# Optimization experiments

Hardware: AMD Instinct MI355X
Metric: run time of the kernel (lower is better)

## Reference

```python
import jax, jax.numpy as jnp
import numpy as np

B, S, D_MODEL = 1, 2048, 2048
N_HEADS, N_KV_HEADS, D_HEAD = 16, 4, 128
ROTARY_DIM, ROTARY_BASE = 128, 10000.0
ATTN_SCALE = float(np.sqrt(D_HEAD))
REPEAT = N_HEADS // N_KV_HEADS


def _sin_cos_rotary(n_ctx, rotary_dim, base):
    # TransformerLens calculate_sin_cos_rotary, rotary_adjacent_pairs=False:
    # freq repeated as 'd -> (2 d)'
    pos = jnp.arange(n_ctx, dtype=jnp.float32)
    dim = jnp.arange(rotary_dim // 2, dtype=jnp.float32)
    freq = base ** (dim / (rotary_dim / 2))
    freq = jnp.concatenate([freq, freq])  # (2 d)
    angles = pos[:, None] / freq[None, :]  # [n_ctx, rotary_dim]
    return jnp.sin(angles), jnp.cos(angles)


def _rotate_every_two_half(x):
    # rotate_half for non-adjacent pairs: [-x2, x1]
    d = x.shape[-1]
    return jnp.concatenate([-x[..., d // 2:], x[..., : d // 2]], axis=-1)


def _apply_rotary(x, sin, cos):
    # x: [batch, pos, head, d_head]; sin/cos: [n_ctx, rotary_dim]
    p = x.shape[1]
    s = sin[:p][:, None, :]  # [pos, 1, rotary_dim]
    c = cos[:p][:, None, :]
    x_rot = x[..., :ROTARY_DIM]
    x_pass = x[..., ROTARY_DIM:]
    x_rotated = x_rot * c + _rotate_every_two_half(x_rot) * s
    return jnp.concatenate([x_rotated, x_pass], axis=-1)


def setup_inputs() -> dict:
    key = jax.random.key(0)
    ks = jax.random.split(key, 10)
    init = 1.0 / np.sqrt(D_MODEL)
    return {
        "query_input": jax.random.normal(ks[0], (B, S, D_MODEL), jnp.float32),
        "key_input": jax.random.normal(ks[1], (B, S, D_MODEL), jnp.float32),
        "value_input": jax.random.normal(ks[2], (B, S, D_MODEL), jnp.float32),
        "W_Q": jax.random.normal(ks[3], (N_HEADS, D_MODEL, D_HEAD), jnp.float32) * init,
        "b_Q": jnp.zeros((N_HEADS, D_HEAD), jnp.float32),
        "W_K": jax.random.normal(ks[4], (N_KV_HEADS, D_MODEL, D_HEAD), jnp.float32) * init,
        "b_K": jnp.zeros((N_KV_HEADS, D_HEAD), jnp.float32),
        "W_V": jax.random.normal(ks[5], (N_KV_HEADS, D_MODEL, D_HEAD), jnp.float32) * init,
        "b_V": jnp.zeros((N_KV_HEADS, D_HEAD), jnp.float32),
        "W_O": jax.random.normal(ks[6], (N_HEADS, D_HEAD, D_MODEL), jnp.float32) * init,
        "b_O": jnp.zeros((D_MODEL,), jnp.float32),
    }


def reference(query_input, key_input, value_input, W_Q, b_Q, W_K, b_K, W_V, b_V, W_O, b_O):
    sin, cos = _sin_cos_rotary(S, ROTARY_DIM, ROTARY_BASE)

    # Projections
    q = jnp.einsum("bpd,hdk->bphk", query_input, W_Q) + b_Q   # [B,S,H,dh]
    k = jnp.einsum("bpd,hdk->bphk", key_input, W_K) + b_K     # [B,S,Hkv,dh]
    v = jnp.einsum("bpd,hdk->bphk", value_input, W_V) + b_V   # [B,S,Hkv,dh]

    # Rotary on q and k (before KV head expansion)
    q = _apply_rotary(q, sin, cos)
    k = _apply_rotary(k, sin, cos)

    # GQA expansion via repeat_interleave on head dim
    k = jnp.repeat(k, REPEAT, axis=2)  # [B,S,H,dh]
    v = jnp.repeat(v, REPEAT, axis=2)

    # Attention scores, causal mask, softmax
    scores = jnp.einsum("bqhd,bkhd->bhqk", q, k) / ATTN_SCALE  # [B,H,S,S]
    causal = jnp.tril(jnp.ones((S, S), dtype=bool))
    scores = jnp.where(causal, scores, jnp.finfo(scores.dtype).min)
    pattern = jax.nn.softmax(scores, axis=-1)

    # Weighted values and output projection
    z = jnp.einsum("bhqk,bkhd->bqhd", pattern, v)              # [B,S,H,dh]
    out = jnp.einsum("bqhd,hdm->bqm", z, W_O) + b_O            # [B,S,D]
    return out
```

## Files before the change

kernel.cpp:

```cpp
#include <hip/hip_runtime.h>
#include <hip/hip_bf16.h>
#include <stdint.h>
#include <math.h>

typedef __bf16 bf16_t;
typedef __attribute__((ext_vector_type(8))) __bf16 bf16x8;
typedef __attribute__((ext_vector_type(4))) __bf16 bf16x4;
typedef __attribute__((ext_vector_type(4))) float f32x4;
typedef __attribute__((ext_vector_type(16))) float f32x16;
typedef unsigned int uint2v __attribute__((ext_vector_type(2)));

static constexpr int S = 2048;
static constexpr int DM = 2048;
static constexpr int NH = 16;
static constexpr int NKV = 4;
static constexpr int DH = 128;

#define MFMA16(a, b, c) __builtin_amdgcn_mfma_f32_16x16x32_bf16((a), (b), (c), 0, 0, 0)
#define MFMA32(a, b, c) __builtin_amdgcn_mfma_f32_32x32x16_bf16((a), (b), (c), 0, 0, 0)

__device__ __forceinline__ void gload_lds16(const void* g, void* l) {
  __builtin_amdgcn_global_load_lds((__attribute__((address_space(1))) void*)(g),
                                   (__attribute__((address_space(3))) void*)(l), 16, 0, 0);
}

template <int N>
__device__ __forceinline__ void wait_vmcnt() {
  asm volatile("s_waitcnt vmcnt(%0)" :: "n"(N) : "memory");
}
__device__ __forceinline__ void wait_lgkm0() {
  asm volatile("s_waitcnt lgkmcnt(0)" ::: "memory");
}

__device__ __forceinline__ unsigned cvtpk(float lo, float hi) {
  unsigned r;
  asm("v_cvt_pk_bf16_f32 %0, %1, %2" : "=v"(r) : "v"(lo), "v"(hi));
  return r;
}
__device__ __forceinline__ void plswap2(unsigned& a, unsigned& b) {
  uint2v r = __builtin_amdgcn_permlane32_swap(a, b, false, false);
  a = r[0]; b = r[1];
}
__device__ __forceinline__ float swapred_max(float x) {
  uint2v r = __builtin_amdgcn_permlane32_swap(__float_as_uint(x), __float_as_uint(x), false, false);
  return fmaxf(__uint_as_float(r[0]), __uint_as_float(r[1]));
}
__device__ __forceinline__ float swapred_sum(float x) {
  uint2v r = __builtin_amdgcn_permlane32_swap(__float_as_uint(x), __float_as_uint(x), false, false);
  return __uint_as_float(r[0]) + __uint_as_float(r[1]);
}
__device__ __forceinline__ bf16x8 packfrag(float a0, float a1, float a2, float a3,
                                           float a4, float a5, float a6, float a7) {
  unsigned w0 = cvtpk(a0, a1), w1 = cvtpk(a2, a3);
  unsigned w2 = cvtpk(a4, a5), w3 = cvtpk(a6, a7);
  plswap2(w0, w2); plswap2(w1, w3);
  union { unsigned u[4]; bf16x8 v; } u;
  u.u[0] = w0; u.u[1] = w1; u.u[2] = w2; u.u[3] = w3;
  return u.v;
}

__device__ const unsigned char attn_map[51] = {
  120,121,122,123,124, 112,113,114,115,116, 104,105,106,107, 96,97,98,99,
  88,89,90,91, 80,81,82, 72,73,74, 64,65,66, 56,57, 48,49, 40,41, 32, 24, 16,
  108, 83, 58, 33, 8, 125, 100, 75, 50, 25, 0};
__device__ const unsigned char sbase[16] = {0,0,0,0,2,4,6,9,12,15,19,23,27,32,37,42};

__global__ __launch_bounds__(256)
void prep_k(const float* __restrict__ Xq, const float* __restrict__ Xk,
            const float* __restrict__ Xv, const float* __restrict__ WQ,
            const float* __restrict__ WK, const float* __restrict__ WV,
            const float* __restrict__ WO, float2* __restrict__ tab,
            bf16_t* __restrict__ xq, bf16_t* __restrict__ xk, bf16_t* __restrict__ xv,
            bf16_t* __restrict__ wqT, bf16_t* __restrict__ wkT, bf16_t* __restrict__ wvT,
            bf16_t* __restrict__ woT) {
  __shared__ float tile[32][33];
  const int b = blockIdx.x, t = threadIdx.x;
  if (b < 512) {
    int idx = b * 256 + t;
    int p = idx >> 6, j = idx & 63;
    double inv = exp2(-(double)j * 13.287712379549449 / 64.0);
    double ang = (double)p * inv;
    tab[idx] = make_float2((float)sin(ang), (float)cos(ang));
  } else if (b < 12800) {
    int i = ((b - 512) * 256 + t) * 4;
    const float* in; bf16_t* out; int off;
    if (i < 4194304) { in = Xq; out = xq; off = i; }
    else if (i < 8388608) { in = Xk; out = xk; off = i - 4194304; }
    else { in = Xv; out = xv; off = i - 8388608; }
    f32x4 v = *(const f32x4*)(in + off);
    bf16x4 o;
    o[0] = (bf16_t)v[0]; o[1] = (bf16_t)v[1]; o[2] = (bf16_t)v[2]; o[3] = (bf16_t)v[3];
    *(bf16x4*)(out + off) = o;
  } else if (b < 16896) {
    int b2 = b - 12800;
    int bx = b2 & 3, by = (b2 >> 2) & 63, bz = b2 >> 8;
    int c0 = bx * 32, r0 = by * 32;
    int tx = t & 31, ty = t >> 5;
    const float* src = WQ + (size_t)bz * 2048 * 128;
    #pragma unroll
    for (int j = 0; j < 32; j += 8)
      tile[ty + j][tx] = src[(size_t)(r0 + ty + j) * 128 + c0 + tx];
    __syncthreads();
    #pragma unroll
    for (int j = 0; j < 32; j += 8)
      wqT[(size_t)(bz * 128 + c0 + ty + j) * 2048 + r0 + tx] = (bf16_t)tile[tx][ty + j];
  } else if (b < 18944) {
    int b2 = b - 16896;
    int bx = b2 & 3, by = (b2 >> 2) & 63, bz = b2 >> 8;
    int g = bz & 3;
    const float* in = (bz < 4) ? WK : WV;
    bf16_t* out = (bz < 4) ? wkT : wvT;
    int c0 = bx * 32, r0 = by * 32;
    int tx = t & 31, ty = t >> 5;
    const float* src = in + (size_t)g * 2048 * 128;
    #pragma unroll
    for (int j = 0; j < 32; j += 8)
      tile[ty + j][tx] = src[(size_t)(r0 + ty + j) * 128 + c0 + tx];
    __syncthreads();
    #pragma unroll
    for (int j = 0; j < 32; j += 8)
      out[(size_t)(g * 128 + c0 + ty + j) * 2048 + r0 + tx] = (bf16_t)tile[tx][ty + j];
  } else {
    int b2 = b - 18944;
    int bx = b2 & 63, by = (b2 >> 6) & 3, bz = b2 >> 8;
    int c0 = bx * 32, r0 = by * 32;
    int tx = t & 31, ty = t >> 5;
    const float* src = WO + (size_t)bz * 128 * 2048;
    #pragma unroll
    for (int j = 0; j < 32; j += 8)
      tile[ty + j][tx] = src[(size_t)(r0 + ty + j) * 2048 + c0 + tx];
    __syncthreads();
    #pragma unroll
    for (int j = 0; j < 32; j += 8)
      woT[(size_t)(c0 + ty + j) * 2048 + bz * 128 + r0 + tx] = (bf16_t)tile[tx][ty + j];
  }
}

__global__ void rope_qk_k(bf16_t* __restrict__ Qb, bf16_t* __restrict__ Kb,
                          const float2* __restrict__ tab, float qscale) {
  int tid = blockIdx.x * 256 + threadIdx.x;
  int row = tid >> 4;
  int i = (tid & 15) * 4;
  bf16_t* base; float scale;
  if (row < NH * S) { base = Qb + (size_t)row * DH; scale = qscale; }
  else { base = Kb + (size_t)(row - NH * S) * DH; scale = 1.0f; }
  int p = row & (S - 1);
  bf16x4 lo = *(bf16x4*)(base + i);
  bf16x4 hi = *(bf16x4*)(base + i + 64);
  float4 t0 = *(const float4*)(tab + p * 64 + i);
  float4 t1 = *(const float4*)(tab + p * 64 + i + 2);
  float sv[4] = {t0.x, t0.z, t1.x, t1.z};
  float cv[4] = {t0.y, t0.w, t1.y, t1.w};
  bf16x4 nlo, nhi;
  #pragma unroll
  for (int j = 0; j < 4; ++j) {
    float a = (float)lo[j], b = (float)hi[j];
    nlo[j] = (bf16_t)((a * cv[j] - b * sv[j]) * scale);
    nhi[j] = (bf16_t)((b * cv[j] + a * sv[j]) * scale);
  }
  *(bf16x4*)(base + i) = nlo;
  *(bf16x4*)(base + i + 64) = nhi;
}

__global__ __launch_bounds__(256)
void proj_gemm_k(const bf16_t* __restrict__ xq, const bf16_t* __restrict__ xk,
                 const bf16_t* __restrict__ xv, const bf16_t* __restrict__ wqT,
                 const bf16_t* __restrict__ wkT, const bf16_t* __restrict__ wvT,
                 const float* __restrict__ bQ, const float* __restrict__ bK,
                 const float* __restrict__ bV, bf16_t* __restrict__ Qb,
                 bf16_t* __restrict__ Kb, bf16_t* __restrict__ Vt) {
  const int b = blockIdx.x;
  const int xcd = b & 7, idx = b >> 3;
  const int nb = (xcd & 3) * 12 + idx % 12;
  const int m0 = ((xcd >> 2) * 8 + idx / 12) * 128;
  const bf16_t* A; const bf16_t* B; const float* bias; bf16_t* dst; int ncol0;
  bool vmode = false;
  if (nb < 32)      { A = xq; B = wqT; bias = bQ; dst = Qb; ncol0 = nb * 64; }
  else if (nb < 40) { A = xk; B = wkT; bias = bK; dst = Kb; ncol0 = (nb - 32) * 64; }
  else              { A = xv; B = wvT; bias = bV; dst = Vt; ncol0 = (nb - 40) * 64; vmode = true; }
  const int K = 2048;
  const int t = threadIdx.x;
  const int lane = t & 63, w = t >> 6;
  const int l15 = lane & 15, lg = lane >> 4;
  const int wr = (w >> 1) * 64, wc = (w & 1) * 32;

  __shared__ bf16_t lA[2][128 * 64];
  __shared__ bf16_t lB[2][64 * 64];

  f32x4 acc[4][2] = {};
  const int srow = t >> 3;
  const int sslot = t & 7;

  auto stage = [&](int buf, int kt) {
    #pragma unroll
    for (int i = 0; i < 4; ++i) {
      int row = i * 32 + srow;
      int ss = sslot ^ (row & 7);
      gload_lds16(A + (size_t)(m0 + row) * K + kt * 64 + ss * 8,
                  (void*)(&lA[buf][0] + i * 2048 + t * 8));
    }
    #pragma unroll
    for (int i = 0; i < 2; ++i) {
      int row = i * 32 + srow;
      int ss = sslot ^ (row & 7);
      gload_lds16(B + (size_t)(ncol0 + row) * K + kt * 64 + ss * 8,
                  (void*)(&lB[buf][0] + i * 2048 + t * 8));
    }
  };

  const int nk = K >> 6;
  stage(0, 0);
  for (int kt = 0; kt < nk; ++kt) {
    const int cur = kt & 1;
    if (kt + 1 < nk) {
      stage(cur ^ 1, kt + 1);
      wait_vmcnt<6>();
    } else {
      wait_vmcnt<0>();
    }
    __builtin_amdgcn_s_barrier();
    #pragma unroll
    for (int kk = 0; kk < 2; ++kk) {
      bf16x8 af[4], bfv[2];
      #pragma unroll
      for (int f = 0; f < 4; ++f) {
        int row = wr + f * 16 + l15;
        int slot = kk * 4 + lg;
        af[f] = *(const bf16x8*)(&lA[cur][0] + row * 64 + ((slot ^ (row & 7)) * 8));
      }
      #pragma unroll
      for (int f = 0; f < 2; ++f) {
        int row = wc + f * 16 + l15;
        int slot = kk * 4 + lg;
        bfv[f] = *(const bf16x8*)(&lB[cur][0] + row * 64 + ((slot ^ (row & 7)) * 8));
      }
      #pragma unroll
      for (int fm = 0; fm < 4; ++fm)
        #pragma unroll
        for (int fn = 0; fn < 2; ++fn)
          acc[fm][fn] = MFMA16(af[fm], bfv[fn], acc[fm][fn]);
    }
    wait_lgkm0();
    __builtin_amdgcn_s_barrier();
  }

  #pragma unroll
  for (int fm = 0; fm < 4; ++fm) {
    int rowb = m0 + wr + fm * 16 + lg * 4;
    #pragma unroll
    for (int fn = 0; fn < 2; ++fn) {
      int col = ncol0 + wc + fn * 16 + l15;
      float bb = bias[col];
      if (vmode) {
        bf16x4 pk;
        #pragma unroll
        for (int r = 0; r < 4; ++r) pk[r] = (bf16_t)(acc[fm][fn][r] + bb);
        *(bf16x4*)(dst + (size_t)col * S + rowb) = pk;
      } else {
        #pragma unroll
        for (int r = 0; r < 4; ++r) {
          float v = acc[fm][fn][r] + bb;
          dst[((size_t)(col >> 7) * S + (rowb + r)) * DH + (col & 127)] = (bf16_t)v;
        }
      }
    }
  }
}

__global__ __launch_bounds__(256)
void gemm_o_k(const bf16_t* __restrict__ A, const bf16_t* __restrict__ B,
              const float* __restrict__ bias, float* __restrict__ Cout) {
  const int b = blockIdx.x;
  const int xcd = b & 7, idx = b >> 3;
  const int ncol0 = ((xcd & 3) * 8 + (idx & 7)) * 64;
  const int m0 = (((xcd >> 2) * 8) + (idx >> 3)) * 128;
  const int K = 2048;
  const int t = threadIdx.x;
  const int lane = t & 63, w = t >> 6;
  const int l15 = lane & 15, lg = lane >> 4;
  const int wr = (w >> 1) * 64, wc = (w & 1) * 32;

  __shared__ bf16_t lA[2][128 * 64];
  __shared__ bf16_t lB[2][64 * 64];

  f32x4 acc[4][2] = {};
  const int srow = t >> 3;
  const int sslot = t & 7;

  auto stage = [&](int buf, int kt) {
    #pragma unroll
    for (int i = 0; i < 4; ++i) {
      int row = i * 32 + srow;
      int ss = sslot ^ (row & 7);
      gload_lds16(A + (size_t)(m0 + row) * K + kt * 64 + ss * 8,
                  (void*)(&lA[buf][0] + i * 2048 + t * 8));
    }
    #pragma unroll
    for (int i = 0; i < 2; ++i) {
      int row = i * 32 + srow;
      int ss = sslot ^ (row & 7);
      gload_lds16(B + (size_t)(ncol0 + row) * K + kt * 64 + ss * 8,
                  (void*)(&lB[buf][0] + i * 2048 + t * 8));
    }
  };

  const int nk = K >> 6;
  stage(0, 0);
  for (int kt = 0; kt < nk; ++kt) {
    const int cur = kt & 1;
    if (kt + 1 < nk) {
      stage(cur ^ 1, kt + 1);
      wait_vmcnt<6>();
    } else {
      wait_vmcnt<0>();
    }
    __builtin_amdgcn_s_barrier();
    #pragma unroll
    for (int kk = 0; kk < 2; ++kk) {
      bf16x8 af[4], bfv[2];
      #pragma unroll
      for (int f = 0; f < 4; ++f) {
        int row = wr + f * 16 + l15;
        int slot = kk * 4 + lg;
        af[f] = *(const bf16x8*)(&lA[cur][0] + row * 64 + ((slot ^ (row & 7)) * 8));
      }
      #pragma unroll
      for (int f = 0; f < 2; ++f) {
        int row = wc + f * 16 + l15;
        int slot = kk * 4 + lg;
        bfv[f] = *(const bf16x8*)(&lB[cur][0] + row * 64 + ((slot ^ (row & 7)) * 8));
      }
      #pragma unroll
      for (int fm = 0; fm < 4; ++fm)
        #pragma unroll
        for (int fn = 0; fn < 2; ++fn)
          acc[fm][fn] = MFMA16(af[fm], bfv[fn], acc[fm][fn]);
    }
    wait_lgkm0();
    __builtin_amdgcn_s_barrier();
  }

  #pragma unroll
  for (int fm = 0; fm < 4; ++fm) {
    int rowb = m0 + wr + fm * 16 + lg * 4;
    #pragma unroll
    for (int fn = 0; fn < 2; ++fn) {
      int col = ncol0 + wc + fn * 16 + l15;
      float bb = bias[col];
      #pragma unroll
      for (int r = 0; r < 4; ++r)
        Cout[(size_t)(rowb + r) * DM + col] = acc[fm][fn][r] + bb;
    }
  }
}

__global__ __launch_bounds__(256, 2)
void attn_k(const bf16_t* __restrict__ Q, const bf16_t* __restrict__ K,
            const bf16_t* __restrict__ Vt, bf16_t* __restrict__ Z,
            bf16_t* __restrict__ Opart, float* __restrict__ mpart,
            float* __restrict__ lpart) {
  const int bid = blockIdx.x;
  const int h = bid & 15;
  const int g = bid >> 4;
  const int code = attn_map[g];
  const int qb = code >> 3, ci = code & 7;
  const bool split = qb >= 3;
  const int it0 = 3 * ci;
  const int itend = (3 * ci + 2 < qb) ? (3 * ci + 2) : qb;
  const int q0 = qb * 128;
  const int hkv = h >> 2;
  const int t = threadIdx.x;
  const int lane = t & 63, w = t >> 6;
  const int l31 = lane & 31, hi = lane >> 5;
  const int qrow = q0 + w * 32 + l31;

  __shared__ bf16_t lK[128 * 128];
  __shared__ bf16_t lV[128 * 128];

  bf16x8 qf[8];
  #pragma unroll
  for (int j = 0; j < 8; ++j)
    qf[j] = *(const bf16x8*)(Q + ((size_t)h * S + qrow) * DH + j * 16 + hi * 8);

  auto stageKV = [&](int it) {
    #pragma unroll
    for (int i = 0; i < 8; ++i) {
      int row = i * 16 + (t >> 4);
      int ss = (t & 15) ^ (row & 15);
      gload_lds16(K + ((size_t)hkv * S + it * 128 + row) * DH + ss * 8,
                  (void*)(lK + i * 2048 + t * 8));
    }
    #pragma unroll
    for (int i = 0; i < 8; ++i) {
      int row = i * 16 + (t >> 4);
      int ss = (t & 15) ^ (row & 15);
      gload_lds16(Vt + ((size_t)hkv * DH + row) * S + it * 128 + ss * 8,
                  (void*)(lV + i * 2048 + t * 8));
    }
  };

  f32x16 oacc0 = {}, oacc1 = {}, oacc2 = {}, oacc3 = {};
  float m_run = -3.0e3f, l_run = 0.f;
  const int msk = l31 & 15;
  const bf16_t* kb0 = lK + l31 * 128;
  const bf16_t* vb0 = lV + l31 * 128;

  for (int it = it0; it <= itend; ++it) {
    __builtin_amdgcn_s_barrier();
    stageKV(it);
    wait_vmcnt<8>();
    __builtin_amdgcn_s_barrier();

    f32x16 s0 = {}, s1 = {}, s2 = {}, s3 = {};
    __builtin_amdgcn_s_setprio(1);
    #pragma unroll
    for (int j = 0; j < 8; ++j) {
      int so = ((j * 2 + hi) ^ msk) * 8;
      bf16x8 k0 = *(const bf16x8*)(kb0 + so);
      bf16x8 k1 = *(const bf16x8*)(kb0 + 32 * 128 + so);
      bf16x8 k2 = *(const bf16x8*)(kb0 + 64 * 128 + so);
      bf16x8 k3 = *(const bf16x8*)(kb0 + 96 * 128 + so);
      s0 = MFMA32(k0, qf[j], s0);
      s1 = MFMA32(k1, qf[j], s1);
      s2 = MFMA32(k2, qf[j], s2);
      s3 = MFMA32(k3, qf[j], s3);
    }
    __builtin_amdgcn_s_setprio(0);

    if (it == qb) {
#define MASKG(SN, N) { \
      _Pragma("unroll") \
      for (int r = 0; r < 16; ++r) { \
        int key = it * 128 + (N) * 32 + (r & 3) + 8 * (r >> 2) + 4 * hi; \
        if (key > qrow) SN[r] = -1e30f; \
      } }
      MASKG(s0, 0) MASKG(s1, 1) MASKG(s2, 2) MASKG(s3, 3)
#undef MASKG
    }

    float mxa = fmaxf(fmaxf(s0[0], s1[0]), fmaxf(s2[0], s3[0]));
    float mxb = fmaxf(fmaxf(s0[1], s1[1]), fmaxf(s2[1], s3[1]));
    float mxc = fmaxf(fmaxf(s0[2], s1[2]), fmaxf(s2[2], s3[2]));
    float mxd = fmaxf(fmaxf(s0[3], s1[3]), fmaxf(s2[3], s3[3]));
    #pragma unroll
    for (int r = 4; r < 16; r += 4) {
      mxa = fmaxf(fmaxf(mxa, fmaxf(s0[r], s1[r])), fmaxf(s2[r], s3[r]));
      mxb = fmaxf(fmaxf(mxb, fmaxf(s0[r+1], s1[r+1])), fmaxf(s2[r+1], s3[r+1]));
      mxc = fmaxf(fmaxf(mxc, fmaxf(s0[r+2], s1[r+2])), fmaxf(s2[r+2], s3[r+2]));
      mxd = fmaxf(fmaxf(mxd, fmaxf(s0[r+3], s1[r+3])), fmaxf(s2[r+3], s3[r+3]));
    }
    float mfull = swapred_max(fmaxf(fmaxf(mxa, mxb), fmaxf(mxc, mxd)));

    float m_new, alpha;
    bool nore = __all(mfull - m_run <= 8.0f);
    if (nore) { m_new = m_run; alpha = 1.0f; }
    else { m_new = fmaxf(m_run, mfull); alpha = exp2f(m_run - m_new); }

    float psa = 0.f, psb = 0.f, psc = 0.f, psd = 0.f;
#define EXPG(SN) { \
    _Pragma("unroll") \
    for (int r = 0; r < 16; r += 4) { \
      SN[r] = exp2f(SN[r] - m_new); psa += SN[r]; \
      SN[r+1] = exp2f(SN[r+1] - m_new); psb += SN[r+1]; \
      SN[r+2] = exp2f(SN[r+2] - m_new); psc += SN[r+2]; \
      SN[r+3] = exp2f(SN[r+3] - m_new); psd += SN[r+3]; \
    } }
    EXPG(s0) EXPG(s1) EXPG(s2) EXPG(s3)
#undef EXPG
    float lt = swapred_sum((psa + psb) + (psc + psd));
    l_run = l_run * alpha + lt;
    m_run = m_new;

    if (!nore) {
      #pragma unroll
      for (int r = 0; r < 16; ++r) {
        int qs = (r & 3) + 8 * (r >> 2) + 4 * hi;
        float ar = __shfl(alpha, qs);
        oacc0[r] *= ar; oacc1[r] *= ar; oacc2[r] *= ar; oacc3[r] *= ar;
      }
    }

    bf16x8 pa[8];
    pa[0] = packfrag(s0[0], s0[1], s0[2], s0[3], s0[4], s0[5], s0[6], s0[7]);
    pa[1] = packfrag(s0[8], s0[9], s0[10], s0[11], s0[12], s0[13], s0[14], s0[15]);
    pa[2] = packfrag(s1[0], s1[1], s1[2], s1[3], s1[4], s1[5], s1[6], s1[7]);
    pa[3] = packfrag(s1[8], s1[9], s1[10], s1[11], s1[12], s1[13], s1[14], s1[15]);
    pa[4] = packfrag(s2[0], s2[1], s2[2], s2[3], s2[4], s2[5], s2[6], s2[7]);
    pa[5] = packfrag(s2[8], s2[9], s2[10], s2[11], s2[12], s2[13], s2[14], s2[15]);
    pa[6] = packfrag(s3[0], s3[1], s3[2], s3[3], s3[4], s3[5], s3[6], s3[7]);
    pa[7] = packfrag(s3[8], s3[9], s3[10], s3[11], s3[12], s3[13], s3[14], s3[15]);

    wait_vmcnt<0>();
    __builtin_amdgcn_s_barrier();

    __builtin_amdgcn_s_setprio(1);
    #pragma unroll
    for (int ks = 0; ks < 8; ++ks) {
      int so = ((ks * 2 + hi) ^ msk) * 8;
      bf16x8 v0 = *(const bf16x8*)(vb0 + so);
      bf16x8 v1 = *(const bf16x8*)(vb0 + 32 * 128 + so);
      bf16x8 v2 = *(const bf16x8*)(vb0 + 64 * 128 + so);
      bf16x8 v3 = *(const bf16x8*)(vb0 + 96 * 128 + so);
      oacc0 = MFMA32(pa[ks], v0, oacc0);
      oacc1 = MFMA32(pa[ks], v1, oacc1);
      oacc2 = MFMA32(pa[ks], v2, oacc2);
      oacc3 = MFMA32(pa[ks], v3, oacc3);
    }
    __builtin_amdgcn_s_setprio(0);
    wait_lgkm0();
  }

  if (!split) {
    float linv = 1.0f / l_run;
    #pragma unroll
    for (int r = 0; r < 16; ++r) {
      int qs = (r & 3) + 8 * (r >> 2) + 4 * hi;
      float lv = __shfl(linv, qs);
      int qg = q0 + w * 32 + qs;
      bf16_t* zp = Z + (size_t)qg * DM + h * DH + l31;
      zp[0]  = (bf16_t)(oacc0[r] * lv);
      zp[32] = (bf16_t)(oacc1[r] * lv);
      zp[64] = (bf16_t)(oacc2[r] * lv);
      zp[96] = (bf16_t)(oacc3[r] * lv);
    }
  } else {
    const int slot = h * 48 + sbase[qb] + ci;
    bf16_t* Op = Opart + (size_t)slot * 16384;
    #pragma unroll
    for (int r = 0; r < 16; ++r) {
      int qs = (r & 3) + 8 * (r >> 2) + 4 * hi;
      bf16_t* op = Op + (w * 32 + qs) * 128 + l31;
      op[0]  = (bf16_t)oacc0[r];
      op[32] = (bf16_t)oacc1[r];
      op[64] = (bf16_t)oacc2[r];
      op[96] = (bf16_t)oacc3[r];
    }
    if (lane < 32) {
      mpart[slot * 128 + w * 32 + l31] = m_run;
      lpart[slot * 128 + w * 32 + l31] = l_run;
    }
  }
}

__global__ void combine_k(const bf16_t* __restrict__ Opart, const float* __restrict__ mpart,
                          const float* __restrict__ lpart, bf16_t* __restrict__ Z) {
  int tid = blockIdx.x * 256 + threadIdx.x;
  int d4 = tid & 31;
  int q = (tid >> 5) & 127;
  int u = tid >> 12;
  int h = u / 13;
  int qb = 3 + (u - h * 13);
  int nc = (qb + 3) / 3;
  int slot0 = h * 48 + sbase[qb];
  float M = -3.0e3f;
  for (int c = 0; c < nc; ++c) M = fmaxf(M, mpart[(slot0 + c) * 128 + q]);
  float L = 0.f;
  float o0 = 0.f, o1 = 0.f, o2 = 0.f, o3 = 0.f;
  for (int c = 0; c < nc; ++c) {
    float a = exp2f(mpart[(slot0 + c) * 128 + q] - M);
    L += a * lpart[(slot0 + c) * 128 + q];
    bf16x4 ov = *(const bf16x4*)(Opart + (size_t)(slot0 + c) * 16384 + q * 128 + d4 * 4);
    o0 += a * (float)ov[0]; o1 += a * (float)ov[1];
    o2 += a * (float)ov[2]; o3 += a * (float)ov[3];
  }
  float inv = 1.0f / L;
  bf16x4 zv;
  zv[0] = (bf16_t)(o0 * inv); zv[1] = (bf16_t)(o1 * inv);
  zv[2] = (bf16_t)(o2 * inv); zv[3] = (bf16_t)(o3 * inv);
  int qg = qb * 128 + q;
  *(bf16x4*)(Z + (size_t)qg * DM + h * DH + d4 * 4) = zv;
}

extern "C" void kernel_launch(void* const* d_in, const int* in_sizes, int n_in,
                              void* d_out, int out_size, void* d_ws, size_t ws_size,
                              hipStream_t stream) {
  (void)in_sizes; (void)n_in; (void)out_size; (void)ws_size;
  const float* Xq = (const float*)d_in[0];
  const float* Xk = (const float*)d_in[1];
  const float* Xv = (const float*)d_in[2];
  const float* WQ = (const float*)d_in[3];
  const float* bQ = (const float*)d_in[4];
  const float* WK = (const float*)d_in[5];
  const float* bK = (const float*)d_in[6];
  const float* WV = (const float*)d_in[7];
  const float* bV = (const float*)d_in[8];
  const float* WO = (const float*)d_in[9];
  const float* bO = (const float*)d_in[10];

  char* w = (char*)d_ws;
  float2* tab = (float2*)w;
  bf16_t* xq  = (bf16_t*)(w + (1 << 20));
  bf16_t* xk  = xq + 4194304;
  bf16_t* xv  = xk + 4194304;
  bf16_t* wqT = xv + 4194304;
  bf16_t* wkT = wqT + 4194304;
  bf16_t* wvT = wkT + 1048576;
  bf16_t* woT = wvT + 1048576;
  bf16_t* Qb  = woT + 4194304;
  bf16_t* Kb  = Qb + 4194304;
  bf16_t* Vtb = Kb + 1048576;
  bf16_t* Zb  = Vtb + 1048576;
  bf16_t* Opart = xq;
  float* mpart = (float*)tab;
  float* lpart = mpart + 768 * 128;

  prep_k<<<dim3(23040), dim3(256), 0, stream>>>(Xq, Xk, Xv, WQ, WK, WV, WO, tab,
                                                xq, xk, xv, wqT, wkT, wvT, woT);

  proj_gemm_k<<<dim3(768), dim3(256), 0, stream>>>(xq, xk, xv, wqT, wkT, wvT,
                                                   bQ, bK, bV, Qb, Kb, Vtb);

  const float qscale = 1.4426950408889634f / sqrtf(128.0f);
  rope_qk_k<<<dim3(2560), dim3(256), 0, stream>>>(Qb, Kb, tab, qscale);

  attn_k<<<dim3(816), dim3(256), 0, stream>>>(Qb, Kb, Vtb, Zb, Opart, mpart, lpart);
  combine_k<<<dim3(3328), dim3(256), 0, stream>>>(Opart, mpart, lpart, Zb);

  gemm_o_k<<<dim3(512), dim3(256), 0, stream>>>(Zb, woT, bO, (float*)d_out);
}
```

Before: 137.9 us.

## Fuse RoPE into projection GEMM epilogue and split K/V prefetch in attention

```diff
diff --git a/kernel.cpp b/kernel.cpp
--- a/kernel.cpp
+++ b/kernel.cpp
@@ -136,47 +136,24 @@
   }
 }
 
-__global__ void rope_qk_k(bf16_t* __restrict__ Qb, bf16_t* __restrict__ Kb,
-                          const float2* __restrict__ tab, float qscale) {
-  int tid = blockIdx.x * 256 + threadIdx.x;
-  int row = tid >> 4;
-  int i = (tid & 15) * 4;
-  bf16_t* base; float scale;
-  if (row < NH * S) { base = Qb + (size_t)row * DH; scale = qscale; }
-  else { base = Kb + (size_t)(row - NH * S) * DH; scale = 1.0f; }
-  int p = row & (S - 1);
-  bf16x4 lo = *(bf16x4*)(base + i);
-  bf16x4 hi = *(bf16x4*)(base + i + 64);
-  float4 t0 = *(const float4*)(tab + p * 64 + i);
-  float4 t1 = *(const float4*)(tab + p * 64 + i + 2);
-  float sv[4] = {t0.x, t0.z, t1.x, t1.z};
-  float cv[4] = {t0.y, t0.w, t1.y, t1.w};
-  bf16x4 nlo, nhi;
-  #pragma unroll
-  for (int j = 0; j < 4; ++j) {
-    float a = (float)lo[j], b = (float)hi[j];
-    nlo[j] = (bf16_t)((a * cv[j] - b * sv[j]) * scale);
-    nhi[j] = (bf16_t)((b * cv[j] + a * sv[j]) * scale);
-  }
-  *(bf16x4*)(base + i) = nlo;
-  *(bf16x4*)(base + i + 64) = nhi;
-}
-
 __global__ __launch_bounds__(256)
 void proj_gemm_k(const bf16_t* __restrict__ xq, const bf16_t* __restrict__ xk,
                  const bf16_t* __restrict__ xv, const bf16_t* __restrict__ wqT,
                  const bf16_t* __restrict__ wkT, const bf16_t* __restrict__ wvT,
                  const float* __restrict__ bQ, const float* __restrict__ bK,
-                 const float* __restrict__ bV, bf16_t* __restrict__ Qb,
+                 const float* __restrict__ bV, const float2* __restrict__ tab,
+                 float qscale, bf16_t* __restrict__ Qb,
                  bf16_t* __restrict__ Kb, bf16_t* __restrict__ Vt) {
   const int b = blockIdx.x;
   const int xcd = b & 7, idx = b >> 3;
   const int nb = (xcd & 3) * 12 + idx % 12;
   const int m0 = ((xcd >> 2) * 8 + idx / 12) * 128;
-  const bf16_t* A; const bf16_t* B; const float* bias; bf16_t* dst; int ncol0;
+  const bf16_t* A; const bf16_t* B; const float* bias; bf16_t* dst;
+  int ncol0 = 0, hbase = 0, hb = 0;
+  float scale = 1.0f;
   bool vmode = false;
-  if (nb < 32)      { A = xq; B = wqT; bias = bQ; dst = Qb; ncol0 = nb * 64; }
-  else if (nb < 40) { A = xk; B = wkT; bias = bK; dst = Kb; ncol0 = (nb - 32) * 64; }
+  if (nb < 32)      { A = xq; B = wqT; bias = bQ; dst = Qb; hbase = (nb >> 1) * 128; hb = nb & 1; scale = qscale; }
+  else if (nb < 40) { A = xk; B = wkT; bias = bK; dst = Kb; hbase = ((nb - 32) >> 1) * 128; hb = (nb - 32) & 1; }
   else              { A = xv; B = wvT; bias = bV; dst = Vt; ncol0 = (nb - 40) * 64; vmode = true; }
   const int K = 2048;
   const int t = threadIdx.x;
@@ -203,7 +180,9 @@
     for (int i = 0; i < 2; ++i) {
       int row = i * 32 + srow;
       int ss = sslot ^ (row & 7);
-      gload_lds16(B + (size_t)(ncol0 + row) * K + kt * 64 + ss * 8,
+      int grow = vmode ? (ncol0 + row)
+                       : (hbase + hb * 32 + (row >> 1) + 64 * (row & 1));
+      gload_lds16(B + (size_t)grow * K + kt * 64 + ss * 8,
                   (void*)(&lB[buf][0] + i * 2048 + t * 8));
     }
   };
@@ -244,23 +223,39 @@
     __builtin_amdgcn_s_barrier();
   }
 
-  #pragma unroll
-  for (int fm = 0; fm < 4; ++fm) {
-    int rowb = m0 + wr + fm * 16 + lg * 4;
-    #pragma unroll
-    for (int fn = 0; fn < 2; ++fn) {
-      int col = ncol0 + wc + fn * 16 + l15;
-      float bb = bias[col];
-      if (vmode) {
+  if (vmode) {
+    #pragma unroll
+    for (int fm = 0; fm < 4; ++fm) {
+      int rowb = m0 + wr + fm * 16 + lg * 4;
+      #pragma unroll
+      for (int fn = 0; fn < 2; ++fn) {
+        int col = ncol0 + wc + fn * 16 + l15;
+        float bb = bias[col];
         bf16x4 pk;
         #pragma unroll
         for (int r = 0; r < 4; ++r) pk[r] = (bf16_t)(acc[fm][fn][r] + bb);
         *(bf16x4*)(dst + (size_t)col * S + rowb) = pk;
-      } else {
+      }
+    }
+  } else {
+    #pragma unroll
+    for (int fm = 0; fm < 4; ++fm) {
+      int rowb = m0 + wr + fm * 16 + lg * 4;
+      #pragma unroll
+      for (int fn = 0; fn < 2; ++fn) {
+        int tc = wc + fn * 16 + l15;
+        int j = hb * 32 + (tc >> 1);
+        int half = tc & 1;
+        int col = hbase + j + 64 * half;
+        float bb = bias[col];
         #pragma unroll
         for (int r = 0; r < 4; ++r) {
+          int rr = rowb + r;
           float v = acc[fm][fn][r] + bb;
-          dst[((size_t)(col >> 7) * S + (rowb + r)) * DH + (col & 127)] = (bf16_t)v;
+          float o = __shfl_xor(v, 1);
+          float2 sc = tab[rr * 64 + j];
+          float res = half ? (v * sc.y + o * sc.x) : (v * sc.y - o * sc.x);
+          dst[((size_t)(col >> 7) * S + rr) * DH + (col & 127)] = (bf16_t)(res * scale);
         }
       }
     }
@@ -382,7 +377,7 @@
   for (int j = 0; j < 8; ++j)
     qf[j] = *(const bf16x8*)(Q + ((size_t)h * S + qrow) * DH + j * 16 + hi * 8);
 
-  auto stageKV = [&](int it) {
+  auto stageK = [&](int it) {
     #pragma unroll
     for (int i = 0; i < 8; ++i) {
       int row = i * 16 + (t >> 4);
@@ -390,6 +385,8 @@
       gload_lds16(K + ((size_t)hkv * S + it * 128 + row) * DH + ss * 8,
                   (void*)(lK + i * 2048 + t * 8));
     }
+  };
+  auto stageV = [&](int it) {
     #pragma unroll
     for (int i = 0; i < 8; ++i) {
       int row = i * 16 + (t >> 4);
@@ -405,9 +402,10 @@
   const bf16_t* kb0 = lK + l31 * 128;
   const bf16_t* vb0 = lV + l31 * 128;
 
+  stageK(it0);
+  stageV(it0);
+
   for (int it = it0; it <= itend; ++it) {
-    __builtin_amdgcn_s_barrier();
-    stageKV(it);
     wait_vmcnt<8>();
     __builtin_amdgcn_s_barrier();
 
@@ -426,6 +424,9 @@
       s3 = MFMA32(k3, qf[j], s3);
     }
     __builtin_amdgcn_s_setprio(0);
+    wait_lgkm0();
+    __builtin_amdgcn_s_barrier();
+    if (it < itend) stageK(it + 1);
 
     if (it == qb) {
 #define MASKG(SN, N) { \
@@ -490,7 +491,8 @@
     pa[6] = packfrag(s3[0], s3[1], s3[2], s3[3], s3[4], s3[5], s3[6], s3[7]);
     pa[7] = packfrag(s3[8], s3[9], s3[10], s3[11], s3[12], s3[13], s3[14], s3[15]);
 
-    wait_vmcnt<0>();
+    if (it < itend) { wait_vmcnt<8>(); }
+    else            { wait_vmcnt<0>(); }
     __builtin_amdgcn_s_barrier();
 
     __builtin_amdgcn_s_setprio(1);
@@ -508,6 +510,8 @@
     }
     __builtin_amdgcn_s_setprio(0);
     wait_lgkm0();
+    __builtin_amdgcn_s_barrier();
+    if (it < itend) stageV(it + 1);
   }
 
   if (!split) {
@@ -607,11 +611,10 @@
   prep_k<<<dim3(23040), dim3(256), 0, stream>>>(Xq, Xk, Xv, WQ, WK, WV, WO, tab,
                                                 xq, xk, xv, wqT, wkT, wvT, woT);
 
+  const float qscale = 1.4426950408889634f / sqrtf(128.0f);
   proj_gemm_k<<<dim3(768), dim3(256), 0, stream>>>(xq, xk, xv, wqT, wkT, wvT,
-                                                   bQ, bK, bV, Qb, Kb, Vtb);
-
-  const float qscale = 1.4426950408889634f / sqrtf(128.0f);
-  rope_qk_k<<<dim3(2560), dim3(256), 0, stream>>>(Qb, Kb, tab, qscale);
+                                                   bQ, bK, bV, tab, qscale,
+                                                   Qb, Kb, Vtb);
 
   attn_k<<<dim3(816), dim3(256), 0, stream>>>(Qb, Kb, Vtb, Zb, Opart, mpart, lpart);
   combine_k<<<dim3(3328), dim3(256), 0, stream>>>(Opart, mpart, lpart, Zb);
```

Result: no change. 138.4 us, median of 2 (+0.4%).
